# Kernel tuning notes

Measured on AMD Instinct MI355X. Metric: run time of the kernel, lower is better.

Reference implementation:

```python
import jax, jax.numpy as jnp
import numpy as np

N = 2048  # query particles
M = 2048  # total particles in table
D = 7     # pos(3) + feat(3) + flag(1)


def _dense_params(key, din, dout):
    kw, kb = jax.random.split(key)
    w = jax.random.normal(kw, (din, dout), dtype=jnp.float32) / np.sqrt(din)
    b = jax.random.normal(kb, (dout,), dtype=jnp.float32) * 0.01
    return w, b


def setup_inputs() -> dict:
    key = jax.random.key(0)
    ks = jax.random.split(key, 11)
    mask = jax.random.randint(ks[0], (N, M), 0, 2) > 0            # [N, M] bool neighbor mask
    index = jax.random.randint(ks[1], (N,), 0, M)                 # [N] center indices
    data = jax.random.normal(ks[2], (M, D), dtype=jnp.float32)    # [M, 7] particle table
    # fluid branch: input dim 3 + (D-3) + (D-3) = 11
    wf0, bf0 = _dense_params(ks[3], 11, 18)
    wf1, bf1 = _dense_params(ks[4], 18, 9)
    wf2, bf2 = _dense_params(ks[5], 9, 6)
    wf3, bf3 = _dense_params(ks[6], 6, 3)
    # solid branch: input dim 3 + (D-3) = 7
    ws0, bs0 = _dense_params(ks[7], 7, 18)
    ws1, bs1 = _dense_params(ks[8], 18, 9)
    ws2, bs2 = _dense_params(ks[9], 9, 6)
    ws3, bs3 = _dense_params(ks[10], 6, 3)
    return {
        "mask": mask, "index": index, "data": data,
        "wf0": wf0, "bf0": bf0, "wf1": wf1, "bf1": bf1,
        "wf2": wf2, "bf2": bf2, "wf3": wf3, "bf3": bf3,
        "ws0": ws0, "bs0": bs0, "ws1": ws1, "bs1": bs1,
        "ws2": ws2, "bs2": bs2, "ws3": ws3, "bs3": bs3,
    }


def _mlp(x, w0, b0, w1, b1, w2, b2, w3, b3):
    h = jnp.tanh(x @ w0 + b0)
    h = jnp.tanh(h @ w1 + b1)
    h = jnp.tanh(h @ w2 + b2)
    return h @ w3 + b3


def reference(mask, index, data,
              wf0, bf0, wf1, bf1, wf2, bf2, wf3, bf3,
              ws0, bs0, ws1, bs1, ws2, bs2, ws3, bs3):
    center = data[index]                                  # [N, 7]
    rel = data[None, :, :3] - center[:, None, :3]         # [N, M, 3] relative positions
    neigh_rest = jnp.broadcast_to(data[None, :, 3:], (center.shape[0], data.shape[0], 4))
    cent_rest = jnp.broadcast_to(center[:, None, 3:], (center.shape[0], data.shape[0], 4))
    fluid_in = jnp.concatenate([rel, neigh_rest, cent_rest], axis=-1)  # [N, M, 11]
    solid_in = jnp.concatenate([rel, cent_rest], axis=-1)              # [N, M, 7]
    x = _mlp(fluid_in, wf0, bf0, wf1, bf1, wf2, bf2, wf3, bf3)  # [N, M, 3]
    y = _mlp(solid_in, ws0, bs0, ws1, bs1, ws2, bs2, ws3, bs3)  # [N, M, 3]
    flag = data[:, 6]
    fmask = (mask & (flag > 0)[None, :]).astype(x.dtype)  # fluid neighbors
    smask = (mask & (flag < 1)[None, :]).astype(y.dtype)  # solid neighbors
    pred = jnp.einsum('nm,nmd->nd', fmask, x) + jnp.einsum('nm,nmd->nd', smask, y)
    return pred  # [N, 3]
```

## Files before the change

### kernel.cpp

```cpp
#include <hip/hip_runtime.h>

#define NROWS 2048
#define MCOLS 2048

#define OFF_AF 0
#define OFF_AS (OFF_AF + NROWS * 20)
#define OFF_BF (OFF_AS + NROWS * 20)
#define OFF_BS (OFF_BF + NROWS * 20)
#define OFF_WP (OFF_BS + NROWS * 20)
#define OFF_CF (OFF_WP + 512)
#define OFF_CS (OFF_CF + NROWS)
#define OFF_LISTS (OFF_CS + NROWS)
#define LF_CAP ((size_t)NROWS * MCOLS)

#define WP_W1 0
#define WP_B1 162
#define WP_W2 171
#define WP_B2 225
#define WP_W3 231
#define WP_B3 249
#define WP_SOLID 252

#define TANH_K 2.8853900817779268f

__device__ __forceinline__ float tanh_pre(float x) {
    float t = __builtin_amdgcn_exp2f(x);
    return 1.0f - 2.0f * __builtin_amdgcn_rcpf(1.0f + t);
}

__device__ __forceinline__ void eval_regs_ilp(float4 P0, float4 P1, float4 P2,
                                              float4 P3, float2 P4,
                                              const float* __restrict__ Bq,
                                              const float* __restrict__ W,
                                              float& p0, float& p1, float& p2) {
    float h[18];
    h[0]  = tanh_pre(P0.x + Bq[0]);  h[1]  = tanh_pre(P0.y + Bq[1]);
    h[2]  = tanh_pre(P0.z + Bq[2]);  h[3]  = tanh_pre(P0.w + Bq[3]);
    h[4]  = tanh_pre(P1.x + Bq[4]);  h[5]  = tanh_pre(P1.y + Bq[5]);
    h[6]  = tanh_pre(P1.z + Bq[6]);  h[7]  = tanh_pre(P1.w + Bq[7]);
    h[8]  = tanh_pre(P2.x + Bq[8]);  h[9]  = tanh_pre(P2.y + Bq[9]);
    h[10] = tanh_pre(P2.z + Bq[10]); h[11] = tanh_pre(P2.w + Bq[11]);
    h[12] = tanh_pre(P3.x + Bq[12]); h[13] = tanh_pre(P3.y + Bq[13]);
    h[14] = tanh_pre(P3.z + Bq[14]); h[15] = tanh_pre(P3.w + Bq[15]);
    h[16] = tanh_pre(P4.x + Bq[16]); h[17] = tanh_pre(P4.y + Bq[17]);
    asm volatile("" : "+v"(h[0]), "+v"(h[1]), "+v"(h[2]), "+v"(h[3]),
                      "+v"(h[4]), "+v"(h[5]), "+v"(h[6]), "+v"(h[7]),
                      "+v"(h[8]), "+v"(h[9]), "+v"(h[10]), "+v"(h[11]),
                      "+v"(h[12]), "+v"(h[13]), "+v"(h[14]), "+v"(h[15]),
                      "+v"(h[16]), "+v"(h[17]));
    float g[9];
#pragma unroll
    for (int o = 0; o < 9; ++o) g[o] = W[WP_B1 + o];
#pragma unroll
    for (int j = 0; j < 18; ++j) {
        const float a = h[j];
#pragma unroll
        for (int o = 0; o < 9; ++o) g[o] += a * W[WP_W1 + j * 9 + o];
    }
#pragma unroll
    for (int o = 0; o < 9; ++o) g[o] = tanh_pre(g[o]);
    asm volatile("" : "+v"(g[0]), "+v"(g[1]), "+v"(g[2]), "+v"(g[3]),
                      "+v"(g[4]), "+v"(g[5]), "+v"(g[6]), "+v"(g[7]),
                      "+v"(g[8]));
    float q[6];
#pragma unroll
    for (int o = 0; o < 6; ++o) q[o] = W[WP_B2 + o];
#pragma unroll
    for (int j = 0; j < 9; ++j) {
        const float a = g[j];
#pragma unroll
        for (int o = 0; o < 6; ++o) q[o] += a * W[WP_W2 + j * 6 + o];
    }
#pragma unroll
    for (int o = 0; o < 6; ++o) q[o] = tanh_pre(q[o]);
    asm volatile("" : "+v"(q[0]), "+v"(q[1]), "+v"(q[2]), "+v"(q[3]),
                      "+v"(q[4]), "+v"(q[5]));
    float o0 = W[WP_B3 + 0], o1 = W[WP_B3 + 1], o2 = W[WP_B3 + 2];
#pragma unroll
    for (int j = 0; j < 6; ++j) {
        const float a = q[j];
        o0 += a * W[WP_W3 + j * 3 + 0];
        o1 += a * W[WP_W3 + j * 3 + 1];
        o2 += a * W[WP_W3 + j * 3 + 2];
    }
    p0 += o0; p1 += o1; p2 += o2;
}

__device__ __forceinline__ void row_loop_ilp(const float* __restrict__ A,
                                             const unsigned short* __restrict__ lst,
                                             int cnt,
                                             const float* __restrict__ Bq,
                                             const float* __restrict__ W,
                                             int tid,
                                             float& p0, float& p1, float& p2) {
    int i = tid;
    if (i >= cnt) return;
    const float* r = A + (int)lst[i] * 20;
    float4 P0 = *(const float4*)(r);
    float4 P1 = *(const float4*)(r + 4);
    float4 P2 = *(const float4*)(r + 8);
    float4 P3 = *(const float4*)(r + 12);
    float2 P4 = *(const float2*)(r + 16);
    for (;;) {
        const int inext = i + 256;
        const bool more = inext < cnt;
        const float* rn = A + (int)lst[more ? inext : i] * 20;
        const float4 N0 = *(const float4*)(rn);
        const float4 N1 = *(const float4*)(rn + 4);
        const float4 N2 = *(const float4*)(rn + 8);
        const float4 N3 = *(const float4*)(rn + 12);
        const float2 N4 = *(const float2*)(rn + 16);
        eval_regs_ilp(P0, P1, P2, P3, P4, Bq, W, p0, p1, p2);
        if (!more) break;
        P0 = N0; P1 = N1; P2 = N2; P3 = N3; P4 = N4;
        i = inext;
    }
}

__global__ void prep_kernel(const int* __restrict__ index,
                            const float* __restrict__ data,
                            const float* __restrict__ wf0, const float* __restrict__ bf0,
                            const float* __restrict__ sw0, const float* __restrict__ sb0,
                            const float* __restrict__ wf1, const float* __restrict__ bf1,
                            const float* __restrict__ wf2, const float* __restrict__ bf2,
                            const float* __restrict__ wf3, const float* __restrict__ bf3,
                            const float* __restrict__ sw1, const float* __restrict__ sb1,
                            const float* __restrict__ sw2, const float* __restrict__ sb2,
                            const float* __restrict__ sw3, const float* __restrict__ sb3,
                            float* __restrict__ wsp) {
    int i = blockIdx.x * blockDim.x + threadIdx.x;
    if (i < NROWS) {
        float d[7], cen[7];
#pragma unroll
        for (int c = 0; c < 7; ++c) d[c] = data[i * 7 + c];
        int ci = index[i];
#pragma unroll
        for (int c = 0; c < 7; ++c) cen[c] = data[ci * 7 + c];
#pragma unroll
        for (int j = 0; j < 18; ++j) {
            float af = 0.f;
#pragma unroll
            for (int c = 0; c < 7; ++c) af += d[c] * wf0[c * 18 + j];
            float as = d[0] * sw0[0 * 18 + j] + d[1] * sw0[1 * 18 + j] + d[2] * sw0[2 * 18 + j];
            float bf = bf0[j], bs = sb0[j];
#pragma unroll
            for (int c = 0; c < 3; ++c) bf -= cen[c] * wf0[c * 18 + j];
#pragma unroll
            for (int c = 0; c < 4; ++c) bf += cen[3 + c] * wf0[(7 + c) * 18 + j];
#pragma unroll
            for (int c = 0; c < 3; ++c) bs -= cen[c] * sw0[c * 18 + j];
#pragma unroll
            for (int c = 0; c < 4; ++c) bs += cen[3 + c] * sw0[(3 + c) * 18 + j];
            wsp[OFF_AF + i * 20 + j] = af * TANH_K;
            wsp[OFF_AS + i * 20 + j] = as * TANH_K;
            wsp[OFF_BF + i * 20 + j] = bf * TANH_K;
            wsp[OFF_BS + i * 20 + j] = bs * TANH_K;
        }
        wsp[OFF_AF + i * 20 + 18] = 0.f; wsp[OFF_AF + i * 20 + 19] = 0.f;
        wsp[OFF_AS + i * 20 + 18] = 0.f; wsp[OFF_AS + i * 20 + 19] = 0.f;
        wsp[OFF_BF + i * 20 + 18] = 0.f; wsp[OFF_BF + i * 20 + 19] = 0.f;
        wsp[OFF_BS + i * 20 + 18] = 0.f; wsp[OFF_BS + i * 20 + 19] = 0.f;
    }
    if (blockIdx.x == 0) {
        int t = threadIdx.x;
        float* wp = wsp + OFF_WP;
        for (int k = t; k < 162; k += 256) wp[WP_W1 + k] = wf1[k] * TANH_K;
        for (int k = t; k < 9;   k += 256) wp[WP_B1 + k] = bf1[k] * TANH_K;
        for (int k = t; k < 54;  k += 256) wp[WP_W2 + k] = wf2[k] * TANH_K;
        for (int k = t; k < 6;   k += 256) wp[WP_B2 + k] = bf2[k] * TANH_K;
        for (int k = t; k < 18;  k += 256) wp[WP_W3 + k] = wf3[k];
        for (int k = t; k < 3;   k += 256) wp[WP_B3 + k] = bf3[k];
        for (int k = t; k < 162; k += 256) wp[WP_SOLID + WP_W1 + k] = sw1[k] * TANH_K;
        for (int k = t; k < 9;   k += 256) wp[WP_SOLID + WP_B1 + k] = sb1[k] * TANH_K;
        for (int k = t; k < 54;  k += 256) wp[WP_SOLID + WP_W2 + k] = sw2[k] * TANH_K;
        for (int k = t; k < 6;   k += 256) wp[WP_SOLID + WP_B2 + k] = sb2[k] * TANH_K;
        for (int k = t; k < 18;  k += 256) wp[WP_SOLID + WP_W3 + k] = sw3[k];
        for (int k = t; k < 3;   k += 256) wp[WP_SOLID + WP_B3 + k] = sb3[k];
    }
}

__global__ __launch_bounds__(256)
void compact_kernel(const int* __restrict__ mask,
                    const float* __restrict__ data,
                    float* __restrict__ wsp) {
    const int lane = threadIdx.x & 63;
    const int n = blockIdx.x * 4 + (threadIdx.x >> 6);
    int* counts_f = (int*)(wsp + OFF_CF);
    int* counts_s = (int*)(wsp + OFF_CS);
    unsigned short* lf = (unsigned short*)(wsp + OFF_LISTS) + (size_t)n * MCOLS;
    unsigned short* ls = lf + LF_CAP;
    const int* mrow = mask + (size_t)n * MCOLS;
    int bf = 0, bs = 0;
    const unsigned long long ltmask = (1ull << lane) - 1ull;
#pragma unroll 1
    for (int it = 0; it < MCOLS / 64; ++it) {
        const int m = it * 64 + lane;
        const int mk = mrow[m];
        const float flag = data[m * 7 + 6];
        const bool af = mk && (flag > 0.f);
        const bool as = mk && (flag < 1.f);
        const unsigned long long balf = __ballot(af);
        const unsigned long long bals = __ballot(as);
        if (af) lf[bf + __popcll(balf & ltmask)] = (unsigned short)m;
        if (as) ls[bs + __popcll(bals & ltmask)] = (unsigned short)m;
        bf += __popcll(balf);
        bs += __popcll(bals);
    }
    if (lane == 0) { counts_f[n] = bf; counts_s[n] = bs; }
}

__global__ __launch_bounds__(256, 4)
void main_ilp(const float* __restrict__ wsp, float* __restrict__ out) {
    const int n = blockIdx.x;
    const int tid = threadIdx.x;
    __shared__ float red[3][4];
    const float* __restrict__ W  = wsp + OFF_WP;
    const float* __restrict__ Bf = wsp + OFF_BF + n * 20;
    const float* __restrict__ Bs = wsp + OFF_BS + n * 20;
    const int cf = ((const int*)(wsp + OFF_CF))[n];
    const int cs = ((const int*)(wsp + OFF_CS))[n];
    const unsigned short* lf = (const unsigned short*)(wsp + OFF_LISTS) + (size_t)n * MCOLS;
    const unsigned short* ls = lf + LF_CAP;

    float p0 = 0.f, p1 = 0.f, p2 = 0.f;
    row_loop_ilp(wsp + OFF_AF, lf, cf, Bf, W, tid, p0, p1, p2);
    row_loop_ilp(wsp + OFF_AS, ls, cs, Bs, W + WP_SOLID, tid, p0, p1, p2);

#pragma unroll
    for (int off = 32; off > 0; off >>= 1) {
        p0 += __shfl_xor(p0, off, 64);
        p1 += __shfl_xor(p1, off, 64);
        p2 += __shfl_xor(p2, off, 64);
    }
    const int wid = tid >> 6;
    if ((tid & 63) == 0) { red[0][wid] = p0; red[1][wid] = p1; red[2][wid] = p2; }
    __syncthreads();
    if (tid == 0) {
        float a0 = 0.f, a1 = 0.f, a2 = 0.f;
#pragma unroll
        for (int w = 0; w < 4; ++w) { a0 += red[0][w]; a1 += red[1][w]; a2 += red[2][w]; }
        out[n * 3 + 0] = a0; out[n * 3 + 1] = a1; out[n * 3 + 2] = a2;
    }
}

extern "C" void kernel_launch(void* const* d_in, const int* in_sizes, int n_in,
                              void* d_out, int out_size, void* d_ws, size_t ws_size,
                              hipStream_t stream) {
    const int*   mask  = (const int*)d_in[0];
    const int*   index = (const int*)d_in[1];
    const float* data  = (const float*)d_in[2];
    const float* wf0   = (const float*)d_in[3];
    const float* bf0   = (const float*)d_in[4];
    const float* wf1   = (const float*)d_in[5];
    const float* bf1   = (const float*)d_in[6];
    const float* wf2   = (const float*)d_in[7];
    const float* bf2   = (const float*)d_in[8];
    const float* wf3   = (const float*)d_in[9];
    const float* bf3   = (const float*)d_in[10];
    const float* sw0   = (const float*)d_in[11];
    const float* sb0   = (const float*)d_in[12];
    const float* sw1   = (const float*)d_in[13];
    const float* sb1   = (const float*)d_in[14];
    const float* sw2   = (const float*)d_in[15];
    const float* sb2   = (const float*)d_in[16];
    const float* sw3   = (const float*)d_in[17];
    const float* sb3   = (const float*)d_in[18];
    float* wsp = (float*)d_ws;
    float* out = (float*)d_out;

    prep_kernel<<<dim3(8), dim3(256), 0, stream>>>(
        index, data, wf0, bf0, sw0, sb0, wf1, bf1, wf2, bf2, wf3, bf3,
        sw1, sb1, sw2, sb2, sw3, sb3, wsp);
    compact_kernel<<<dim3(NROWS / 4), dim3(256), 0, stream>>>(mask, data, wsp);
    main_ilp<<<dim3(NROWS), dim3(256), 0, stream>>>(wsp, out);
}
```

Baseline: 69.39 us.

## Fuse neighbor compaction into main kernel using LDS lists and precomputed flag bitmasks

Removes the separate compaction kernel and its global-memory index lists. Prep now writes per-64-particle ballot bitmasks of the fluid and solid flags. Each main block compacts its own mask row into shared memory, builds a prefix over the per-wave segments, and then runs the MLP loops reading indices from LDS. This saves one launch and the global write and read-back of about 16 MB of ushort lists. In exchange it uses 16 KB of LDS per block, which may limit occupancy, and adds block-level syncs before the compute starts.

Result: faster. 60.25 us (-13.2%).

```diff
diff --git a/kernel.cpp b/kernel.cpp
--- a/kernel.cpp
+++ b/kernel.cpp
@@ -8,10 +8,8 @@
 #define OFF_BF (OFF_AS + NROWS * 20)
 #define OFF_BS (OFF_BF + NROWS * 20)
 #define OFF_WP (OFF_BS + NROWS * 20)
-#define OFF_CF (OFF_WP + 512)
-#define OFF_CS (OFF_CF + NROWS)
-#define OFF_LISTS (OFF_CS + NROWS)
-#define LF_CAP ((size_t)NROWS * MCOLS)
+#define OFF_FB (OFF_WP + 512)
+#define OFF_SB (OFF_FB + 64)
 
 #define WP_W1 0
 #define WP_B1 162
@@ -87,7 +85,7 @@
 }
 
 __device__ __forceinline__ void row_loop_ilp(const float* __restrict__ A,
-                                             const unsigned short* __restrict__ lst,
+                                             const unsigned short* lst,
                                              int cnt,
                                              const float* __restrict__ Bq,
                                              const float* __restrict__ W,
@@ -160,6 +158,12 @@
         wsp[OFF_AS + i * 20 + 18] = 0.f; wsp[OFF_AS + i * 20 + 19] = 0.f;
         wsp[OFF_BF + i * 20 + 18] = 0.f; wsp[OFF_BF + i * 20 + 19] = 0.f;
         wsp[OFF_BS + i * 20 + 18] = 0.f; wsp[OFF_BS + i * 20 + 19] = 0.f;
+        const unsigned long long bal_f = __ballot(d[6] > 0.f);
+        const unsigned long long bal_s = __ballot(d[6] < 1.f);
+        if ((i & 63) == 0) {
+            ((unsigned long long*)(wsp + OFF_FB))[i >> 6] = bal_f;
+            ((unsigned long long*)(wsp + OFF_SB))[i >> 6] = bal_s;
+        }
     }
     if (blockIdx.x == 0) {
         int t = threadIdx.x;
@@ -179,52 +183,65 @@
     }
 }
 
-__global__ __launch_bounds__(256)
-void compact_kernel(const int* __restrict__ mask,
-                    const float* __restrict__ data,
-                    float* __restrict__ wsp) {
-    const int lane = threadIdx.x & 63;
-    const int n = blockIdx.x * 4 + (threadIdx.x >> 6);
-    int* counts_f = (int*)(wsp + OFF_CF);
-    int* counts_s = (int*)(wsp + OFF_CS);
-    unsigned short* lf = (unsigned short*)(wsp + OFF_LISTS) + (size_t)n * MCOLS;
-    unsigned short* ls = lf + LF_CAP;
-    const int* mrow = mask + (size_t)n * MCOLS;
-    int bf = 0, bs = 0;
-    const unsigned long long ltmask = (1ull << lane) - 1ull;
-#pragma unroll 1
-    for (int it = 0; it < MCOLS / 64; ++it) {
-        const int m = it * 64 + lane;
-        const int mk = mrow[m];
-        const float flag = data[m * 7 + 6];
-        const bool af = mk && (flag > 0.f);
-        const bool as = mk && (flag < 1.f);
-        const unsigned long long balf = __ballot(af);
-        const unsigned long long bals = __ballot(as);
-        if (af) lf[bf + __popcll(balf & ltmask)] = (unsigned short)m;
-        if (as) ls[bs + __popcll(bals & ltmask)] = (unsigned short)m;
-        bf += __popcll(balf);
-        bs += __popcll(bals);
-    }
-    if (lane == 0) { counts_f[n] = bf; counts_s[n] = bs; }
-}
-
 __global__ __launch_bounds__(256, 4)
-void main_ilp(const float* __restrict__ wsp, float* __restrict__ out) {
+void main_fused(const int* __restrict__ mask,
+                const float* __restrict__ wsp,
+                float* __restrict__ out) {
+    __shared__ unsigned short segF[2048], segS[2048];
+    __shared__ unsigned short flatF[2048], flatS[2048];
+    __shared__ int wc[8];
+    __shared__ int pc[10];
+    __shared__ float red[3][4];
     const int n = blockIdx.x;
     const int tid = threadIdx.x;
-    __shared__ float red[3][4];
+    const int w = tid >> 6, lane = tid & 63;
+    const int* mrow = mask + (size_t)n * MCOLS;
+    const unsigned long long* fb = (const unsigned long long*)(wsp + OFF_FB);
+    const unsigned long long* sbits = (const unsigned long long*)(wsp + OFF_SB);
+    const unsigned long long ltm = (1ull << lane) - 1ull;
+
+    int cf = 0, cs = 0;
+#pragma unroll 1
+    for (int it = 0; it < 8; ++it) {
+        const int m = w * 512 + it * 64 + lane;
+        const int widx = w * 8 + it;
+        const int mk = mrow[m];
+        const bool af = mk && ((fb[widx] >> lane) & 1ull);
+        const bool as = mk && ((sbits[widx] >> lane) & 1ull);
+        const unsigned long long bf_ = __ballot(af);
+        const unsigned long long bs_ = __ballot(as);
+        if (af) segF[w * 512 + cf + __popcll(bf_ & ltm)] = (unsigned short)m;
+        if (as) segS[w * 512 + cs + __popcll(bs_ & ltm)] = (unsigned short)m;
+        cf += __popcll(bf_);
+        cs += __popcll(bs_);
+    }
+    if (lane == 0) { wc[w] = cf; wc[4 + w] = cs; }
+    __syncthreads();
+    if (tid == 0) {
+        int aF = 0, aS = 0;
+#pragma unroll
+        for (int k = 0; k < 4; ++k) {
+            pc[k] = aF; aF += wc[k];
+            pc[5 + k] = aS; aS += wc[4 + k];
+        }
+        pc[4] = aF; pc[9] = aS;
+    }
+    __syncthreads();
+    {
+        const int baseF = pc[w], cntF = wc[w];
+        for (int k = lane; k < cntF; k += 64) flatF[baseF + k] = segF[w * 512 + k];
+        const int baseS = pc[5 + w], cntS = wc[4 + w];
+        for (int k = lane; k < cntS; k += 64) flatS[baseS + k] = segS[w * 512 + k];
+    }
+    __syncthreads();
+    const int cftot = pc[4], cstot = pc[9];
+
     const float* __restrict__ W  = wsp + OFF_WP;
     const float* __restrict__ Bf = wsp + OFF_BF + n * 20;
     const float* __restrict__ Bs = wsp + OFF_BS + n * 20;
-    const int cf = ((const int*)(wsp + OFF_CF))[n];
-    const int cs = ((const int*)(wsp + OFF_CS))[n];
-    const unsigned short* lf = (const unsigned short*)(wsp + OFF_LISTS) + (size_t)n * MCOLS;
-    const unsigned short* ls = lf + LF_CAP;
-
     float p0 = 0.f, p1 = 0.f, p2 = 0.f;
-    row_loop_ilp(wsp + OFF_AF, lf, cf, Bf, W, tid, p0, p1, p2);
-    row_loop_ilp(wsp + OFF_AS, ls, cs, Bs, W + WP_SOLID, tid, p0, p1, p2);
+    row_loop_ilp(wsp + OFF_AF, flatF, cftot, Bf, W, tid, p0, p1, p2);
+    row_loop_ilp(wsp + OFF_AS, flatS, cstot, Bs, W + WP_SOLID, tid, p0, p1, p2);
 
 #pragma unroll
     for (int off = 32; off > 0; off >>= 1) {
@@ -232,13 +249,12 @@
         p1 += __shfl_xor(p1, off, 64);
         p2 += __shfl_xor(p2, off, 64);
     }
-    const int wid = tid >> 6;
-    if ((tid & 63) == 0) { red[0][wid] = p0; red[1][wid] = p1; red[2][wid] = p2; }
+    if (lane == 0) { red[0][w] = p0; red[1][w] = p1; red[2][w] = p2; }
     __syncthreads();
     if (tid == 0) {
         float a0 = 0.f, a1 = 0.f, a2 = 0.f;
 #pragma unroll
-        for (int w = 0; w < 4; ++w) { a0 += red[0][w]; a1 += red[1][w]; a2 += red[2][w]; }
+        for (int k = 0; k < 4; ++k) { a0 += red[0][k]; a1 += red[1][k]; a2 += red[2][k]; }
         out[n * 3 + 0] = a0; out[n * 3 + 1] = a1; out[n * 3 + 2] = a2;
     }
 }
@@ -271,6 +287,5 @@
     prep_kernel<<<dim3(8), dim3(256), 0, stream>>>(
         index, data, wf0, bf0, sw0, sb0, wf1, bf1, wf2, bf2, wf3, bf3,
         sw1, sb1, sw2, sb2, sw3, sb3, wsp);
-    compact_kernel<<<dim3(NROWS / 4), dim3(256), 0, stream>>>(mask, data, wsp);
-    main_ilp<<<dim3(NROWS), dim3(256), 0, stream>>>(wsp, out);
-}
+    main_fused<<<dim3(NROWS), dim3(256), 0, stream>>>(mask, wsp, out);
+}
```
